# Kernel tuning notes

Measured on AMD Instinct MI355X. Metric: run time of the kernel, lower is better.

## Reference

```python
import jax, jax.numpy as jnp
import numpy as np

NUM_CODES = 4096
CODE_DIM = 512
BETA = 0.25
EPS = 1e-5


def setup_inputs() -> dict:
    key = jax.random.key(0)
    k1, k2 = jax.random.split(key)
    z_e = jax.random.normal(k1, (8, 2048, CODE_DIM), dtype=jnp.float32)
    mask = jnp.ones((8, 2048), dtype=bool)
    # torch init: uniform(-1/num_codes, 1/num_codes)
    codebook = jax.random.uniform(
        k2, (NUM_CODES, CODE_DIM), dtype=jnp.float32,
        minval=-1.0 / NUM_CODES, maxval=1.0 / NUM_CODES)
    return {"z_e": z_e, "mask": mask, "codebook": codebook}


def _l2norm(x, eps=1e-8):
    # matches F.normalize: x / norm.clamp_min(eps)
    n = jnp.sqrt(jnp.sum(x * x, axis=-1, keepdims=True))
    return x / jnp.maximum(n, eps)


def reference(z_e, mask, codebook):
    """Eval-mode forward of VectorQuantizerEMA (no gumbel noise, no code
    dropout, no EMA/restart buffer updates -- those only run in training)."""
    B, L, C = z_e.shape
    K = codebook.shape[0]
    flat = z_e.reshape(-1, C)                      # [N, C]
    fmask = mask.reshape(-1)                       # [N] bool
    mf = fmask.astype(flat.dtype)

    # cosine similarity logits  [N, K]
    logits = _l2norm(flat) @ _l2norm(codebook).T
    logits = jnp.clip(
        jnp.nan_to_num(logits, nan=0.0, posinf=1e9, neginf=-1e9), -60.0, 60.0)

    hard_idx = jnp.argmax(logits, axis=1)          # [N]

    # hard one-hot quantization == gather of codebook rows; masked rows -> 0
    z_q_flat = codebook[hard_idx] * mf[:, None]
    z_q = z_q_flat.reshape(B, L, C)
    z_q_st = z_e + jax.lax.stop_gradient(z_q - z_e)

    m = mf.reshape(B, L, 1)
    valid = jnp.maximum(jnp.sum(m), 1.0)
    commitment_loss = jnp.sum((z_q - jax.lax.stop_gradient(z_e)) ** 2 * m) / valid
    vq_loss = BETA * commitment_loss

    # perplexity over valid assignments (bincount)
    counts = jax.ops.segment_sum(mf, hard_idx, num_segments=K)
    probs = counts / (jnp.sum(counts) + EPS)
    perplexity = jnp.exp(-jnp.sum(probs * jnp.log(probs + EPS)))

    return (z_q, z_q_st, hard_idx.reshape(B, L), vq_loss,
            commitment_loss, perplexity)
```

## Files before the change

kernel.cpp:

```cpp
#include <hip/hip_runtime.h>

typedef __attribute__((ext_vector_type(4))) float f32x4_t;
typedef __attribute__((ext_vector_type(8))) short bf16x8_t;

#define NROWS 16384
#define NCODES 4096
#define DIM 512
#define DELTA 0.005f
#define MAXC 16

#define WS_A      0u
#define WS_B      16777216u
#define WS_TOPE   20971520u
#define WS_COUNTS 37748736u
#define WS_FLAGS  37765120u
#define WS_IDX    37765184u
#define WS_ITEMS  37830720u
#define WS_CPART  39206976u
#define WS_GPART  39239744u

#define OUT_ZQ      0
#define OUT_ZQST    8388608
#define OUT_IDX     16777216
#define OUT_VQ      16793600
#define OUT_COMMIT  16793601
#define OUT_PERP    16793602

__device__ __forceinline__ unsigned short f2bf(float x) {
  unsigned u = __builtin_bit_cast(unsigned, x);
  unsigned r = (u + 0x7FFFu + ((u >> 16) & 1u)) >> 16;
  return (unsigned short)r;
}
__device__ __forceinline__ unsigned hz(unsigned x) {
  return (x - 0x01010101u) & ~x & 0x80808080u;
}
__device__ __forceinline__ unsigned swz64(int r, int u) {
  return (unsigned)(r * 128 + ((u ^ (r & 7)) << 4));
}

__global__ void prep_kernel(const float* __restrict__ z, const float* __restrict__ cb,
                            unsigned char* __restrict__ Aws, unsigned char* __restrict__ Bws,
                            unsigned* __restrict__ counts) {
  if (blockIdx.x < 17) {
    int zi = blockIdx.x * 256 + threadIdx.x;
    if (zi < 4100) counts[zi] = 0;
  }
  const int wv = threadIdx.x >> 6, lane = threadIdx.x & 63;
  const int row = blockIdx.x * 4 + wv;
  if (row >= NROWS + NCODES) return;
  const bool isA = row < NROWS;
  const int lrow = isA ? row : row - NROWS;
  const float* src = (isA ? z : cb) + (size_t)lrow * DIM;
  f32x4_t a = *(const f32x4_t*)(src + lane * 8);
  f32x4_t b = *(const f32x4_t*)(src + lane * 8 + 4);
  double s = 0.0;
#pragma unroll
  for (int e = 0; e < 4; ++e) s += (double)a[e] * a[e] + (double)b[e] * b[e];
#pragma unroll
  for (int off = 1; off < 64; off <<= 1) s += __shfl_xor(s, off);
  const float inv = (float)(1.0 / fmax(sqrt(s), 1e-8));
  union { unsigned short u[8]; uint4 v; } H;
#pragma unroll
  for (int e = 0; e < 4; ++e) {
    H.u[e] = f2bf(a[e] * inv);
    H.u[4 + e] = f2bf(b[e] * inv);
  }
  const int tb = lrow >> 7, rr = lrow & 127;
  const int st = lane >> 3, u = lane & 7;
  unsigned char* chunk = (isA ? Aws : Bws) + ((size_t)tb * 8 + st) * 16384;
  *(uint4*)(chunk + swz64(rr, u)) = H.v;
}

__global__ __launch_bounds__(256, 4) void gemm_p1_kernel(
    const unsigned char* __restrict__ Aws, const unsigned char* __restrict__ Bws,
    float4* __restrict__ topE) {
  __align__(16) __shared__ unsigned char smem[32768];

  const int tid = threadIdx.x;
  const int bid = blockIdx.x;
  const int xcd = bid & 7, q = bid >> 3;
  const int rb = xcd * 16 + (q >> 3), cg = q & 7;
  const int wave = tid >> 6, lane = tid & 63;
  const int wr = wave >> 1, wc = wave & 1;
  const int kg = lane >> 4, lr = lane & 15;

  const unsigned char* Ach = Aws + (size_t)rb * 8 * 16384;

  auto issue_stage = [&](const unsigned char* Asrc, const unsigned char* Bsrc) {
#pragma unroll
    for (int i = 0; i < 8; ++i) {
      const int j = wave * 8 + i;
      const unsigned char* sp = (j < 16) ? (Asrc + (size_t)j * 1024 + lane * 16)
                                         : (Bsrc + (size_t)(j - 16) * 1024 + lane * 16);
      __builtin_amdgcn_global_load_lds(
          (const __attribute__((address_space(1))) void*)sp,
          (__attribute__((address_space(3))) void*)(smem + j * 1024), 16, 0, 0);
    }
  };

  for (int ct = 0; ct < 4; ++ct) {
    const int ctile = cg * 4 + ct;
    const int code0 = ctile * 128;
    const unsigned char* Bch = Bws + (size_t)ctile * 8 * 16384;

    f32x4_t acc[4][4];
#pragma unroll
    for (int m = 0; m < 4; ++m)
#pragma unroll
      for (int n = 0; n < 4; ++n) acc[m][n] = (f32x4_t){0.f, 0.f, 0.f, 0.f};

    for (int st = 0; st < 8; ++st) {
      if (!(st == 0 && ct > 0))
        issue_stage(Ach + (size_t)st * 16384, Bch + (size_t)st * 16384);
      __syncthreads();

#pragma unroll
      for (int kk = 0; kk < 2; ++kk) {
        bf16x8_t ah[4], bh[4];
        const int u = kk * 4 + kg;
#pragma unroll
        for (int m = 0; m < 4; ++m) {
          const int r = wr * 64 + m * 16 + lr;
          ah[m] = *(const bf16x8_t*)(smem + swz64(r, u));
        }
#pragma unroll
        for (int n = 0; n < 4; ++n) {
          const int r = wc * 64 + n * 16 + lr;
          bh[n] = *(const bf16x8_t*)(smem + 16384 + swz64(r, u));
        }
#pragma unroll
        for (int m = 0; m < 4; ++m)
#pragma unroll
          for (int n = 0; n < 4; ++n)
            acc[m][n] = __builtin_amdgcn_mfma_f32_16x16x32_bf16(ah[m], bh[n], acc[m][n], 0, 0, 0);
      }
      __syncthreads();
    }

    if (ct < 3)
      issue_stage(Ach, Bws + (size_t)(ctile + 1) * 8 * 16384);

#pragma unroll
    for (int m = 0; m < 4; ++m) {
#pragma unroll
      for (int j = 0; j < 4; ++j) {
        float v1 = -3e38f, v2 = -3e38f; int i1 = 0, i2 = 0;
#pragma unroll
        for (int n = 0; n < 4; ++n) {
          float v = acc[m][n][j];
          int gc = code0 + wc * 64 + n * 16 + lr;
          if (v > v1) { v2 = v1; i2 = i1; v1 = v; i1 = gc; }
          else if (v > v2) { v2 = v; i2 = gc; }
        }
#pragma unroll
        for (int mask = 1; mask <= 8; mask <<= 1) {
          float ov1 = __shfl_xor(v1, mask); int oi1 = __shfl_xor(i1, mask);
          float ov2 = __shfl_xor(v2, mask); int oi2 = __shfl_xor(i2, mask);
          bool of = (ov1 > v1) || (ov1 == v1 && oi1 < i1);
          float w1 = of ? ov1 : v1;  int k1 = of ? oi1 : i1;
          float lv = of ? v1 : ov1;  int li = of ? i1 : oi1;
          float sv = of ? ov2 : v2;  int si = of ? oi2 : i2;
          bool lw = (lv > sv) || (lv == sv && li < si);
          v1 = w1; i1 = k1;
          v2 = lw ? lv : sv; i2 = lw ? li : si;
        }
        if (lr == m * 4 + j) {
          const int row = rb * 128 + wr * 64 + m * 16 + kg * 4 + j;
          topE[(size_t)row * 64 + ctile * 2 + wc] =
              make_float4(v1, __builtin_bit_cast(float, i1), v2, __builtin_bit_cast(float, i2));
        }
      }
    }
  }
}

__global__ void resolve_kernel(const uint4* __restrict__ mk, const float4* __restrict__ topE,
                               int* __restrict__ idxf, int* __restrict__ items,
                               unsigned* __restrict__ flags) {
  if (blockIdx.x == 0) {
    unsigned f = 0;
    for (int i = threadIdx.x; i < 1024; i += 256) {
      uint4 v = mk[i];
      f |= hz(v.x) | hz(v.y) | hz(v.z) | hz(v.w);
    }
    if (f) atomicOr(&flags[0], 1u);
  }
  const int row = blockIdx.x * 256 + threadIdx.x;
  if (row >= NROWS) return;
  const float4* e = topE + (size_t)row * 64;
  float V1 = -3e38f; int I1 = 0;
  for (int h = 0; h < 64; ++h) {
    float4 qv = e[h];
    if (qv.x > V1) { V1 = qv.x; I1 = __builtin_bit_cast(int, qv.y); }
  }
  const float T = V1 - 2.0f * DELTA;
  unsigned long long smask = 0ull;
  int cnt = 0; int cid[MAXC];
  for (int h = 0; h < 64; ++h) {
    float4 qv = e[h];
    if (qv.x >= T) {
      if (cnt < MAXC) cid[cnt++] = __builtin_bit_cast(int, qv.y);
      else smask |= 1ull << h;
    }
    if (qv.z >= T) smask |= 1ull << h;
  }
  idxf[row] = I1;
  if (cnt >= 2 || smask != 0ull) {
    unsigned s = atomicAdd(&flags[1], 1u);
    if (s < NROWS) {
      int* o = items + (size_t)s * 20;
      o[0] = row; o[1] = cnt;
      o[2] = (int)(unsigned)(smask & 0xFFFFFFFFull);
      o[3] = (int)(unsigned)(smask >> 32);
#pragma unroll
      for (int c2 = 0; c2 < MAXC; ++c2) o[4 + c2] = (c2 < cnt) ? cid[c2] : 0;
    }
  }
}

__global__ void groupscan_part(const float* __restrict__ z, const float* __restrict__ cb,
                               const int* __restrict__ items, const unsigned* __restrict__ flags,
                               double2* __restrict__ gpart) {
  const int lane = threadIdx.x & 63;
  const int gw = (blockIdx.x * 256 + threadIdx.x) >> 6;
  const int nwaves = gridDim.x * 4;
  unsigned n = flags[1];
  if (n > (unsigned)NROWS) n = NROWS;
  const unsigned tot = n * 8u;
  for (unsigned u = gw; u < tot; u += nwaves) {
    const unsigned it = u >> 3;
    const int slot = (int)(u & 7u);
    const int* en = items + (size_t)it * 20;
    const int row = en[0], cnt = en[1];
    const unsigned long long smask = ((unsigned long long)(unsigned)en[3] << 32) | (unsigned)en[2];
    const int total = cnt + 64 * __popcll(smask);
    double bs = -1e300; int bi = 1 << 30;
    if (slot < total) {
      const float* zr = z + (size_t)row * DIM + lane * 8;
      double zv[8];
#pragma unroll
      for (int j = 0; j < 8; ++j) zv[j] = (double)zr[j];
      auto code_at = [&](int w) -> int {
        if (w < cnt) return en[4 + w];
        const int qq = w - cnt;
        const int gsel = qq >> 6, off = qq & 63;
        unsigned long long m = smask;
        for (int i = 0; i < gsel; ++i) m &= m - 1;
        return (int)__builtin_ctzll(m) * 64 + off;
      };
      auto score2 = [&](int k0, int k1) {
        const float* c0 = cb + (size_t)k0 * DIM + lane * 8;
        const float* c1 = cb + (size_t)((k1 < 0) ? k0 : k1) * DIM + lane * 8;
        double d0 = 0, n0 = 0, d1 = 0, n1 = 0;
#pragma unroll
        for (int j = 0; j < 8; ++j) {
          double a = c0[j]; d0 += zv[j] * a; n0 += a * a;
          double b = c1[j]; d1 += zv[j] * b; n1 += b * b;
        }
#pragma unroll
        for (int off = 1; off < 64; off <<= 1) {
          d0 += __shfl_xor(d0, off); n0 += __shfl_xor(n0, off);
          d1 += __shfl_xor(d1, off); n1 += __shfl_xor(n1, off);
        }
        double s0 = d0 / sqrt(n0);
        if (s0 > bs || (s0 == bs && k0 < bi)) { bs = s0; bi = k0; }
        if (k1 >= 0) {
          double s1 = d1 / sqrt(n1);
          if (s1 > bs || (s1 == bs && k1 < bi)) { bs = s1; bi = k1; }
        }
      };
      int w = slot;
      while (w < total) {
        const int k0 = code_at(w); w += 8;
        const int k1 = (w < total) ? code_at(w) : -1; w += 8;
        score2(k0, k1);
      }
    }
    if (lane == 0) gpart[u] = make_double2(bs, (double)bi);
  }
}

__global__ void groupscan_merge(const double2* __restrict__ gpart, const int* __restrict__ items,
                                const unsigned* __restrict__ flags, int* __restrict__ idxf) {
  unsigned n = flags[1];
  if (n > (unsigned)NROWS) n = NROWS;
  for (unsigned it = blockIdx.x * 256 + threadIdx.x; it < n; it += gridDim.x * 256) {
    double bs = -1e300; int bi = 1 << 30;
#pragma unroll
    for (int s2 = 0; s2 < 8; ++s2) {
      double2 e = gpart[(size_t)it * 8 + s2];
      const int k = (int)e.y;
      if (e.x > bs || (e.x == bs && k < bi)) { bs = e.x; bi = k; }
    }
    if (bi < NCODES) idxf[items[(size_t)it * 20]] = bi;
  }
}

__global__ void outputs_kernel(const float* __restrict__ z, const float* __restrict__ cb,
                               const unsigned char* __restrict__ mask8, const int* __restrict__ mask32,
                               const unsigned* __restrict__ flags, const int* __restrict__ idxf,
                               float* __restrict__ out, unsigned* __restrict__ counts,
                               double* __restrict__ cpart) {
  __shared__ double wsum[4];
  const int wv = threadIdx.x >> 6, lane = threadIdx.x & 63;
  const int row = blockIdx.x * 4 + wv;
  int idx = idxf[row];
  idx = (idx < 0) ? 0 : ((idx > NCODES - 1) ? NCODES - 1 : idx);
  const int mi = flags[0] ? (mask32[row] != 0) : (mask8[row] != 0);
  const float mf = mi ? 1.0f : 0.0f;
  const float* zr = z + (size_t)row * DIM;
  const float* cr = cb + (size_t)idx * DIM;
  double cs = 0.0;
#pragma unroll
  for (int h = 0; h < 2; ++h) {
    const int j = h * 256 + lane * 4;
    f32x4_t c  = *(const f32x4_t*)(cr + j);
    f32x4_t ze = *(const f32x4_t*)(zr + j);
    f32x4_t zq, zs;
#pragma unroll
    for (int e = 0; e < 4; ++e) {
      float qv = c[e] * mf;
      float d = qv - ze[e];
      zq[e] = qv;
      zs[e] = ze[e] + d;
      cs += (double)(d * d) * mf;
    }
    *(f32x4_t*)(out + OUT_ZQ   + (size_t)row * DIM + j) = zq;
    *(f32x4_t*)(out + OUT_ZQST + (size_t)row * DIM + j) = zs;
  }
#pragma unroll
  for (int off = 32; off; off >>= 1) cs += __shfl_down(cs, off);
  if (lane == 0) {
    wsum[wv] = cs;
    out[OUT_IDX + row] = (float)idx;
    if (mi) atomicAdd(&counts[idx], 1u);
  }
  __syncthreads();
  if (threadIdx.x == 0) cpart[blockIdx.x] = wsum[0] + wsum[1] + wsum[2] + wsum[3];
}

__global__ void finalize_kernel(const double* __restrict__ cpart, const unsigned* __restrict__ counts,
                                float* __restrict__ out) {
  __shared__ double sd[256];
  const int t = threadIdx.x;
  double s = 0;
  for (int i = t; i < 4096; i += 256) s += cpart[i];
  sd[t] = s; __syncthreads();
  for (int off = 128; off; off >>= 1) { if (t < off) sd[t] += sd[t + off]; __syncthreads(); }
  const double commit_sum = sd[0];
  __syncthreads();
  double c = 0;
  for (int i = t; i < 4096; i += 256) c += (double)counts[i];
  sd[t] = c; __syncthreads();
  for (int off = 128; off; off >>= 1) { if (t < off) sd[t] += sd[t + off]; __syncthreads(); }
  const double totc = sd[0];
  __syncthreads();
  const double denom = totc + 1e-5;
  double ent = 0;
  for (int i = t; i < 4096; i += 256) {
    double p = (double)counts[i] / denom;
    ent -= p * log(p + 1e-5);
  }
  sd[t] = ent; __syncthreads();
  for (int off = 128; off; off >>= 1) { if (t < off) sd[t] += sd[t + off]; __syncthreads(); }
  if (t == 0) {
    const double valid = fmax(totc, 1.0);
    const double commitment = commit_sum / valid;
    out[OUT_VQ]     = (float)(0.25 * commitment);
    out[OUT_COMMIT] = (float)commitment;
    out[OUT_PERP]   = (float)exp(sd[0]);
  }
}

extern "C" void kernel_launch(void* const* d_in, const int* in_sizes, int n_in,
                              void* d_out, int out_size, void* d_ws, size_t ws_size,
                              hipStream_t stream) {
  const float* z  = (const float*)d_in[0];
  const void*  mk = d_in[1];
  const float* cb = (const float*)d_in[2];
  float* out = (float*)d_out;
  char* ws = (char*)d_ws;

  unsigned char* Aws    = (unsigned char*)(ws + WS_A);
  unsigned char* Bws    = (unsigned char*)(ws + WS_B);
  float4*        topE   = (float4*)(ws + WS_TOPE);
  unsigned*      counts = (unsigned*)(ws + WS_COUNTS);
  unsigned*      flags  = (unsigned*)(ws + WS_FLAGS);
  int*           idxf   = (int*)(ws + WS_IDX);
  int*           items  = (int*)(ws + WS_ITEMS);
  double*        cpart  = (double*)(ws + WS_CPART);
  double2*       gpart  = (double2*)(ws + WS_GPART);

  prep_kernel<<<(NROWS + NCODES) / 4, 256, 0, stream>>>(z, cb, Aws, Bws, counts);
  gemm_p1_kernel<<<1024, 256, 0, stream>>>(Aws, Bws, topE);
  resolve_kernel<<<NROWS / 256, 256, 0, stream>>>((const uint4*)mk, topE, idxf, items, flags);
  groupscan_part<<<2048, 256, 0, stream>>>(z, cb, items, flags, gpart);
  groupscan_merge<<<64, 256, 0, stream>>>(gpart, items, flags, idxf);
  outputs_kernel<<<NROWS / 4, 256, 0, stream>>>(z, cb, (const unsigned char*)mk, (const int*)mk,
                                                flags, idxf, out, counts, cpart);
  finalize_kernel<<<1, 256, 0, stream>>>(cpart, counts, out);
}
```

Measured before the change: 299.8 us.

## Accumulate per-lane top-2 across code tiles and shrink cross-lane reduction

The GEMM epilogue now keeps a running per-lane top-1/top-2 over all four code tiles in registers, then does one short two-step shuffle reduction at the end instead of a full 16-lane shuffle reduction after every tile. Each topE entry therefore covers a strided group of 64 codes, so the fallback rescoring maps group bits to code indices through new grp_base/grp_code helpers and drops the second index. The mask scan and flag zeroing move into the prep kernel. In exchange it adds 48 live registers per thread, which may lower occupancy under the launch bounds, and ties the candidate-group layout to the tile mapping.

```diff
diff --git a/kernel.cpp b/kernel.cpp
--- a/kernel.cpp
+++ b/kernel.cpp
@@ -37,13 +37,29 @@
 __device__ __forceinline__ unsigned swz64(int r, int u) {
   return (unsigned)(r * 128 + ((u ^ (r & 7)) << 4));
 }
+__device__ __forceinline__ int grp_base(int g) {
+  return (g >> 3) * 512 + ((g >> 2) & 1) * 64 + (g & 3) * 4;
+}
+__device__ __forceinline__ int grp_code(int cbase, int o) {
+  return cbase + (o >> 4) * 128 + ((o >> 2) & 3) * 16 + (o & 3);
+}
 
 __global__ void prep_kernel(const float* __restrict__ z, const float* __restrict__ cb,
+                            const uint4* __restrict__ mk,
                             unsigned char* __restrict__ Aws, unsigned char* __restrict__ Bws,
-                            unsigned* __restrict__ counts) {
-  if (blockIdx.x < 17) {
-    int zi = blockIdx.x * 256 + threadIdx.x;
-    if (zi < 4100) counts[zi] = 0;
+                            unsigned* __restrict__ counts, unsigned* __restrict__ flags) {
+  if (blockIdx.x < 16) {
+    counts[blockIdx.x * 256 + threadIdx.x] = 0;
+  }
+  if (blockIdx.x == 0) {
+    if (threadIdx.x < 4) flags[threadIdx.x] = 0;
+    __syncthreads();
+    unsigned f = 0;
+    for (int i = threadIdx.x; i < 1024; i += 256) {
+      uint4 v = mk[i];
+      f |= hz(v.x) | hz(v.y) | hz(v.z) | hz(v.w);
+    }
+    if (f) atomicOr(&flags[0], 1u);
   }
   const int wv = threadIdx.x >> 6, lane = threadIdx.x & 63;
   const int row = blockIdx.x * 4 + wv;
@@ -78,8 +94,8 @@
 
   const int tid = threadIdx.x;
   const int bid = blockIdx.x;
-  const int xcd = bid & 7, q = bid >> 3;
-  const int rb = xcd * 16 + (q >> 3), cg = q & 7;
+  const int xcd = bid & 7, q0 = bid >> 3;
+  const int rb = xcd * 16 + (q0 >> 3), cg = q0 & 7;
   const int wave = tid >> 6, lane = tid & 63;
   const int wr = wave >> 1, wc = wave & 1;
   const int kg = lane >> 4, lr = lane & 15;
@@ -98,6 +114,10 @@
     }
   };
 
+  float tv1[16], tv2[16]; int ti1[16];
+#pragma unroll
+  for (int q = 0; q < 16; ++q) { tv1[q] = -3e38f; tv2[q] = -3e38f; ti1[q] = 0; }
+
   for (int ct = 0; ct < 4; ++ct) {
     const int ctile = cg * 4 + ct;
     const int code0 = ctile * 128;
@@ -141,68 +161,66 @@
       issue_stage(Ach, Bws + (size_t)(ctile + 1) * 8 * 16384);
 
 #pragma unroll
-    for (int m = 0; m < 4; ++m) {
+    for (int m = 0; m < 4; ++m)
 #pragma unroll
       for (int j = 0; j < 4; ++j) {
-        float v1 = -3e38f, v2 = -3e38f; int i1 = 0, i2 = 0;
+        const int q = m * 4 + j;
 #pragma unroll
         for (int n = 0; n < 4; ++n) {
           float v = acc[m][n][j];
           int gc = code0 + wc * 64 + n * 16 + lr;
-          if (v > v1) { v2 = v1; i2 = i1; v1 = v; i1 = gc; }
-          else if (v > v2) { v2 = v; i2 = gc; }
-        }
-#pragma unroll
-        for (int mask = 1; mask <= 8; mask <<= 1) {
-          float ov1 = __shfl_xor(v1, mask); int oi1 = __shfl_xor(i1, mask);
-          float ov2 = __shfl_xor(v2, mask); int oi2 = __shfl_xor(i2, mask);
-          bool of = (ov1 > v1) || (ov1 == v1 && oi1 < i1);
-          float w1 = of ? ov1 : v1;  int k1 = of ? oi1 : i1;
-          float lv = of ? v1 : ov1;  int li = of ? i1 : oi1;
-          float sv = of ? ov2 : v2;  int si = of ? oi2 : i2;
-          bool lw = (lv > sv) || (lv == sv && li < si);
-          v1 = w1; i1 = k1;
-          v2 = lw ? lv : sv; i2 = lw ? li : si;
-        }
-        if (lr == m * 4 + j) {
-          const int row = rb * 128 + wr * 64 + m * 16 + kg * 4 + j;
-          topE[(size_t)row * 64 + ctile * 2 + wc] =
-              make_float4(v1, __builtin_bit_cast(float, i1), v2, __builtin_bit_cast(float, i2));
+          if (v > tv1[q]) { tv2[q] = tv1[q]; tv1[q] = v; ti1[q] = gc; }
+          else if (v > tv2[q]) tv2[q] = v;
         }
       }
-    }
-  }
-}
-
-__global__ void resolve_kernel(const uint4* __restrict__ mk, const float4* __restrict__ topE,
-                               int* __restrict__ idxf, int* __restrict__ items,
-                               unsigned* __restrict__ flags) {
-  if (blockIdx.x == 0) {
-    unsigned f = 0;
-    for (int i = threadIdx.x; i < 1024; i += 256) {
-      uint4 v = mk[i];
-      f |= hz(v.x) | hz(v.y) | hz(v.z) | hz(v.w);
-    }
-    if (f) atomicOr(&flags[0], 1u);
-  }
+  }
+
+#pragma unroll
+  for (int m = 0; m < 4; ++m)
+#pragma unroll
+    for (int j = 0; j < 4; ++j) {
+      const int q = m * 4 + j;
+      float v1 = tv1[q], v2 = tv2[q]; int i1 = ti1[q];
+#pragma unroll
+      for (int mask = 1; mask <= 2; mask <<= 1) {
+        float ov1 = __shfl_xor(v1, mask); int oi1 = __shfl_xor(i1, mask);
+        float ov2 = __shfl_xor(v2, mask);
+        bool of = (ov1 > v1) || (ov1 == v1 && oi1 < i1);
+        float w1 = of ? ov1 : v1;  int k1 = of ? oi1 : i1;
+        float lv = of ? v1 : ov1;
+        float sv = of ? ov2 : v2;
+        v1 = w1; i1 = k1;
+        v2 = (lv > sv) ? lv : sv;
+      }
+      if ((lr & 3) == 0) {
+        const int row = rb * 128 + wr * 64 + m * 16 + kg * 4 + j;
+        topE[(size_t)row * 64 + cg * 8 + wc * 4 + (lr >> 2)] =
+            make_float4(v1, __builtin_bit_cast(float, i1), v2, 0.f);
+      }
+    }
+}
+
+__global__ void resolve_kernel(const float4* __restrict__ topE, int* __restrict__ idxf,
+                               int* __restrict__ items, unsigned* __restrict__ flags) {
   const int row = blockIdx.x * 256 + threadIdx.x;
   if (row >= NROWS) return;
   const float4* e = topE + (size_t)row * 64;
-  float V1 = -3e38f; int I1 = 0;
-  for (int h = 0; h < 64; ++h) {
-    float4 qv = e[h];
-    if (qv.x > V1) { V1 = qv.x; I1 = __builtin_bit_cast(int, qv.y); }
+  float V1 = -3e38f; int I1 = 1 << 30;
+  for (int g = 0; g < 64; ++g) {
+    float4 qv = e[g];
+    const int i = __builtin_bit_cast(int, qv.y);
+    if (qv.x > V1 || (qv.x == V1 && i < I1)) { V1 = qv.x; I1 = i; }
   }
   const float T = V1 - 2.0f * DELTA;
   unsigned long long smask = 0ull;
   int cnt = 0; int cid[MAXC];
-  for (int h = 0; h < 64; ++h) {
-    float4 qv = e[h];
+  for (int g = 0; g < 64; ++g) {
+    float4 qv = e[g];
     if (qv.x >= T) {
       if (cnt < MAXC) cid[cnt++] = __builtin_bit_cast(int, qv.y);
-      else smask |= 1ull << h;
-    }
-    if (qv.z >= T) smask |= 1ull << h;
+      else smask |= 1ull << g;
+    }
+    if (qv.z >= T) smask |= 1ull << g;
   }
   idxf[row] = I1;
   if (cnt >= 2 || smask != 0ull) {
@@ -243,10 +261,10 @@
       auto code_at = [&](int w) -> int {
         if (w < cnt) return en[4 + w];
         const int qq = w - cnt;
-        const int gsel = qq >> 6, off = qq & 63;
+        const int gsel = qq >> 6, o = qq & 63;
         unsigned long long m = smask;
         for (int i = 0; i < gsel; ++i) m &= m - 1;
-        return (int)__builtin_ctzll(m) * 64 + off;
+        return grp_code(grp_base((int)__builtin_ctzll(m)), o);
       };
       auto score2 = [&](int k0, int k1) {
         const float* c0 = cb + (size_t)k0 * DIM + lane * 8;
@@ -391,9 +409,10 @@
   double*        cpart  = (double*)(ws + WS_CPART);
   double2*       gpart  = (double2*)(ws + WS_GPART);
 
-  prep_kernel<<<(NROWS + NCODES) / 4, 256, 0, stream>>>(z, cb, Aws, Bws, counts);
+  prep_kernel<<<(NROWS + NCODES) / 4, 256, 0, stream>>>(z, cb, (const uint4*)mk, Aws, Bws,
+                                                        counts, flags);
   gemm_p1_kernel<<<1024, 256, 0, stream>>>(Aws, Bws, topE);
-  resolve_kernel<<<NROWS / 256, 256, 0, stream>>>((const uint4*)mk, topE, idxf, items, flags);
+  resolve_kernel<<<NROWS / 256, 256, 0, stream>>>(topE, idxf, items, flags);
   groupscan_part<<<2048, 256, 0, stream>>>(z, cb, items, flags, gpart);
   groupscan_merge<<<64, 256, 0, stream>>>(gpart, items, flags, idxf);
   outputs_kernel<<<NROWS / 4, 256, 0, stream>>>(z, cb, (const unsigned char*)mk, (const int*)mk,
```

Result: faster. 276.1 us (-7.9%).
